# Optimization experiments

Hardware: AMD Instinct MI355X
Metric: run time of the kernel (lower is better)

## Reference

```python
import jax, jax.numpy as jnp
import numpy as np

B, SE, T, S, D, V = 64, 128, 64, 1024, 1024, 32000


def setup_inputs() -> dict:
    key = jax.random.key(0)
    ks = jax.random.split(key, 24)
    w = lambda k, shp: jax.random.normal(k, shp, jnp.float32) * 0.02
    return {
        "encoder_yts": jax.random.normal(ks[0], (B, SE, S), jnp.float32),
        "encoder_h": jax.random.normal(ks[1], (B, S), jnp.float32),
        "tgt": jax.random.randint(ks[2], (B, T), 0, V),
        "emb": w(ks[3], (V, D)),
        "asi_w": w(ks[4], (S, S)), "asi_b": jnp.zeros((S,), jnp.float32),
        "ayi_w": w(ks[5], (S, S)), "ayi_b": jnp.zeros((S,), jnp.float32),
        "aw_w": w(ks[6], (S, 1)), "aw_b": jnp.zeros((1,), jnp.float32),
        "wf_w": w(ks[7], (S, S)), "wf_b": jnp.zeros((S,), jnp.float32),
        "uf_w": w(ks[8], (D, S)), "uf_b": jnp.zeros((S,), jnp.float32),
        "wi_w": w(ks[9], (S, S)), "wi_b": jnp.zeros((S,), jnp.float32),
        "ui_w": w(ks[10], (D, S)), "ui_b": jnp.zeros((S,), jnp.float32),
        "wo_w": w(ks[11], (S, S)), "wo_b": jnp.zeros((S,), jnp.float32),
        "uo_w": w(ks[12], (D, S)), "uo_b": jnp.zeros((S,), jnp.float32),
        "wc_w": w(ks[13], (S, S)), "wc_b": jnp.zeros((S,), jnp.float32),
        "uc_w": w(ks[14], (D, S)), "uc_b": jnp.zeros((S,), jnp.float32),
        "xh_w": w(ks[15], (S, D)), "xh_b": jnp.zeros((D,), jnp.float32),
        "cls_w": w(ks[16], (D, V)), "cls_b": jnp.zeros((V,), jnp.float32),
    }


def reference(encoder_yts, encoder_h, tgt, emb,
              asi_w, asi_b, ayi_w, ayi_b, aw_w, aw_b,
              wf_w, wf_b, uf_w, uf_b, wi_w, wi_b, ui_w, ui_b,
              wo_w, wo_b, uo_w, uo_b, wc_w, wc_b, uc_w, uc_b,
              xh_w, xh_b, cls_w, cls_b):
    # Teacher-forced decode: xt at step i is the embedding of tgt[:, i].
    # Precompute attention key projection of encoder outputs: [B, SE, S]
    yts_proj = encoder_yts @ ayi_w + ayi_b
    xs = jnp.transpose(emb[tgt], (1, 0, 2))  # [T, B, D]

    def step(st, xt):
        # Additive attention (no tanh, matches source): e_ij = w^T(W si + U y)
        q = st @ asi_w + asi_b                       # [B, S]
        e = ((q[:, None, :] + yts_proj) @ aw_w)[..., 0] + aw_b[0]  # [B, SE]
        attn = jax.nn.softmax(e, axis=-1)            # [B, SE]
        ctx = jnp.einsum('be,bed->bd', attn, encoder_yts)  # [B, S] cell input
        # LSTM cell: note ct_1 is the fresh attention context each step
        ft = jax.nn.sigmoid(st @ wf_w + wf_b + xt @ uf_w + uf_b)
        it = jax.nn.sigmoid(st @ wi_w + wi_b + xt @ ui_w + ui_b)
        ot = jax.nn.sigmoid(st @ wo_w + wo_b + xt @ uo_w + uo_b)
        cbar = jnp.tanh(st @ wc_w + wc_b + xt @ uc_w + uc_b)
        ct = ft * ctx + it * cbar
        ht = ot * jnp.tanh(ct)                       # [B, S] -> next st
        logits = (ht @ xh_w + xh_b) @ cls_w + cls_b  # [B, V]
        pt = jax.nn.softmax(logits, axis=-1)
        return ht, (pt, attn)

    _, (pts, attns) = jax.lax.scan(step, encoder_h, xs)
    # [T,B,V] -> [B,T,V]; [T,B,SE] -> [B,T,SE]
    return jnp.transpose(pts, (1, 0, 2)), jnp.transpose(attns, (1, 0, 2))
```

## Files before the change

kernel.cpp:

```cpp
#include <hip/hip_runtime.h>
#include <cstdint>
#include <cstddef>

#define B_  64
#define SE_ 128
#define T_  64
#define S_  1024
#define D_  1024
#define V_  32000
#define HSLOT 65536ull

typedef __attribute__((ext_vector_type(8))) short bhalf8;
typedef __attribute__((ext_vector_type(4))) float floatx4;

__device__ __forceinline__ float sigmoidf_(float x){ return 1.0f/(1.0f+__expf(-x)); }

__device__ __forceinline__ ushort f2bf(float f){
  uint32_t u = __float_as_uint(f);
  uint32_t r = (u + 0x7fffu + ((u >> 16) & 1u)) >> 16;
  return (ushort)r;
}
__device__ __forceinline__ float bf2f(ushort h){ return __uint_as_float(((uint32_t)h) << 16); }

__device__ __forceinline__ void glds16(const ushort* g, ushort* l){
  __builtin_amdgcn_global_load_lds((const __attribute__((address_space(1))) void*)g,
                                   (__attribute__((address_space(3))) void*)l, 16, 0, 0);
}

__device__ __forceinline__ float waveRedSum(float v){
  #pragma unroll
  for (int off = 32; off; off >>= 1) v += __shfl_down(v, off, 64);
  return v;
}


__global__ void k_attnvec(const float* __restrict__ ayi_w, const float* __restrict__ aw_w,
                          float* __restrict__ v){
  int wave = (blockIdx.x * blockDim.x + threadIdx.x) >> 6;
  int lane = threadIdx.x & 63;
  if (wave >= S_) return;
  const float* row = ayi_w + (size_t)wave * S_;
  float acc = 0.f;
  #pragma unroll 4
  for (int s = lane; s < S_; s += 64) acc += row[s] * aw_w[s];
  acc = waveRedSum(acc);
  if (lane == 0) v[wave] = acc;
}

__global__ void k_scores(const float* __restrict__ yts, const float* __restrict__ v,
                         float* __restrict__ scores){
  int wave = (blockIdx.x * blockDim.x + threadIdx.x) >> 6;
  int lane = threadIdx.x & 63;
  const float* row = yts + (size_t)wave * S_;
  float acc = 0.f;
  #pragma unroll 4
  for (int s = lane; s < S_; s += 64) acc += row[s] * v[s];
  acc = waveRedSum(acc);
  if (lane == 0) scores[wave] = acc;
}

__global__ void k_attn(const float* __restrict__ scores, float* __restrict__ attnw,
                       float* __restrict__ outAttn){
  int b = blockIdx.x;
  int e = threadIdx.x;
  __shared__ float sm[128];
  float x = scores[b*SE_ + e];
  sm[e] = x; __syncthreads();
  #pragma unroll
  for (int off = 64; off; off >>= 1){
    if (e < off) sm[e] = fmaxf(sm[e], sm[e+off]);
    __syncthreads();
  }
  float m = sm[0]; __syncthreads();
  float p = __expf(x - m);
  sm[e] = p; __syncthreads();
  #pragma unroll
  for (int off = 64; off; off >>= 1){
    if (e < off) sm[e] += sm[e+off];
    __syncthreads();
  }
  float a = p / sm[0];
  attnw[b*SE_ + e] = a;
  float* dst = outAttn + (size_t)b * T_ * SE_ + e;
  #pragma unroll 4
  for (int t = 0; t < T_; ++t) dst[t*SE_] = a;
}

__global__ void k_ctx(const float* __restrict__ yts, const float* __restrict__ attnw,
                      float* __restrict__ ctx){
  int idx = blockIdx.x * blockDim.x + threadIdx.x;
  int b = idx >> 10, s = idx & (S_-1);
  const float* base = yts + (size_t)b * SE_ * S_ + s;
  const float* a = attnw + b * SE_;
  float acc = 0.f;
  #pragma unroll 8
  for (int e = 0; e < SE_; ++e) acc += a[e] * base[(size_t)e * S_];
  ctx[idx] = acc;
}


__global__ void k_transcvt(const float* __restrict__ src, ushort* __restrict__ dst,
                           int K, int N){
  __shared__ float t[32][33];
  int n0 = blockIdx.x * 32, k0 = blockIdx.y * 32;
  for (int r = threadIdx.y; r < 32; r += 8)
    t[r][threadIdx.x] = src[(size_t)(k0 + r) * N + n0 + threadIdx.x];
  __syncthreads();
  for (int r = threadIdx.y; r < 32; r += 8)
    dst[(size_t)(n0 + r) * K + k0 + threadIdx.x] = f2bf(t[threadIdx.x][r]);
}

__global__ void k_cvtrep(const float* __restrict__ src, ushort* __restrict__ Hgs){
  int i = blockIdx.x * blockDim.x + threadIdx.x;
  float4 v = ((const float4*)src)[i];
  ushort4 o; o.x = f2bf(v.x); o.y = f2bf(v.y); o.z = f2bf(v.z); o.w = f2bf(v.w);
  #pragma unroll
  for (int g = 0; g < 8; ++g) {
    size_t gbase = (g == 0) ? 0ull : (65ull + (size_t)(g-1)*8ull) * HSLOT;
    ((ushort4*)(Hgs + gbase))[i] = o;
  }
}

__global__ void k_gathercvt(const float* __restrict__ emb, const int* __restrict__ tgt,
                            ushort* __restrict__ Xb){
  int r = blockIdx.x;
  int token = tgt[((r & 63) << 6) + (r >> 6)];
  const float4* src = (const float4*)(emb + (size_t)token * D_);
  ushort* dst = Xb + (size_t)r * D_;
  int i = threadIdx.x;
  float4 v = src[i];
  ushort4 o; o.x = f2bf(v.x); o.y = f2bf(v.y); o.z = f2bf(v.z); o.w = f2bf(v.w);
  ((ushort4*)dst)[i] = o;
}

__global__ void k_packbias(const float* __restrict__ wb0, const float* __restrict__ wb1,
                           const float* __restrict__ wb2, const float* __restrict__ wb3,
                           const float* __restrict__ ub0, const float* __restrict__ ub1,
                           const float* __restrict__ ub2, const float* __restrict__ ub3,
                           float* __restrict__ dst){
  int col = blockIdx.x * blockDim.x + threadIdx.x;
  int g = col >> 10, s = col & 1023;
  const float* wb = (g==0) ? wb0 : (g==1) ? wb1 : (g==2) ? wb2 : wb3;
  const float* ub = (g==0) ? ub0 : (g==1) ? ub1 : (g==2) ? ub2 : ub3;
  dst[col] = wb[s] + ub[s];
}

template<int OUT_MODE>
__global__ __launch_bounds__(256) void k_mfma_gemm(
    const ushort* __restrict__ A, const ushort* __restrict__ BT,
    const float* __restrict__ bias, void* __restrict__ C, int M, int N)
{
  __shared__ ushort As[128*32];
  __shared__ ushort Bs[128*32];
  const int tid = threadIdx.x;
  const int lane = tid & 63, w = tid >> 6;
  const int nwg = gridDim.x * gridDim.y;
  const int L = blockIdx.y * gridDim.x + blockIdx.x;
  const int logical = (L & 7) * (nwg >> 3) + (L >> 3);
  const int by = logical / gridDim.x;
  const int bx = logical - by * gridDim.x;
  const int m0 = by * 128, n0 = bx * 128;
  const int wr = (w >> 1) * 64, wc = (w & 1) * 64;

  const int cr = (lane >> 2);
  const int ck = (lane & 3) * 8;
  const ushort* gA0 = A  + (size_t)(m0 + (2*w)*16   + cr) * 1024 + ck;
  const ushort* gA1 = A  + (size_t)(m0 + (2*w+1)*16 + cr) * 1024 + ck;
  const ushort* gB0 = BT + (size_t)(n0 + (2*w)*16   + cr) * 1024 + ck;
  const ushort* gB1 = BT + (size_t)(n0 + (2*w+1)*16 + cr) * 1024 + ck;
  ushort* lA0 = As + (2*w)*512;   ushort* lA1 = As + (2*w+1)*512;
  ushort* lB0 = Bs + (2*w)*512;   ushort* lB1 = Bs + (2*w+1)*512;

  floatx4 acc[4][4] = {};

  for (int kt = 0; kt < 1024; kt += 32) {
    glds16(gA0 + kt, lA0); glds16(gA1 + kt, lA1);
    glds16(gB0 + kt, lB0); glds16(gB1 + kt, lB1);
    __syncthreads();
    bhalf8 a[4], b[4];
    #pragma unroll
    for (int f = 0; f < 4; ++f) {
      a[f] = *(const bhalf8*)&As[(wr + f*16 + (lane & 15)) * 32 + (lane >> 4) * 8];
      b[f] = *(const bhalf8*)&Bs[(wc + f*16 + (lane & 15)) * 32 + (lane >> 4) * 8];
    }
    #pragma unroll
    for (int i = 0; i < 4; ++i)
      #pragma unroll
      for (int j = 0; j < 4; ++j)
        acc[i][j] = __builtin_amdgcn_mfma_f32_16x16x32_bf16(a[i], b[j], acc[i][j], 0, 0, 0);
    __syncthreads();
  }

  const int crow = (lane >> 4) * 4, ccol = lane & 15;
  #pragma unroll
  for (int i = 0; i < 4; ++i) {
    #pragma unroll
    for (int j = 0; j < 4; ++j) {
      int row = m0 + wr + i*16 + crow;
      int col = n0 + wc + j*16 + ccol;
      float bv = bias ? bias[col] : 0.f;
      #pragma unroll
      for (int r = 0; r < 4; ++r) {
        float v = acc[i][j][r] + bv;
        if (OUT_MODE == 0) {
          ((float*)C)[(size_t)(row + r) * N + col] = v;
        } else if (OUT_MODE == 1) {
          int rr = row + r;
          ((float*)C)[(size_t)(((rr & 63) << 6) + (rr >> 6)) * N + col] = v;
        } else {
          ((ushort*)C)[(size_t)(row + r) * N + col] = f2bf(v);
        }
      }
    }
  }
}

__global__ __launch_bounds__(512) void k_recur(
    const ushort* __restrict__ WT, const ushort* __restrict__ preb,
    const float* __restrict__ ctx, ushort* __restrict__ Hgs,
    uint* __restrict__ ready, uint* __restrict__ cnt)
{
  extern __shared__ char smem[];
  float* gbuf = (float*)smem;
  __shared__ uint sgrp, srank;
  const int tid = threadIdx.x, lane = tid & 63, w = tid >> 6;

  if (tid == 0) {
    uint xcc;
    asm volatile("s_getreg_b32 %0, hwreg(HW_REG_XCC_ID, 0, 32)" : "=s"(xcc));
    xcc &= 7u;
    sgrp = xcc;
    srank = atomicAdd(&cnt[xcc], 1u) & 31u;
  }
  __syncthreads();
  const int grp = (int)sgrp, r = (int)srank;
  const size_t gbase = (grp == 0) ? 0ull : (65ull + (size_t)(grp-1)*8ull) * HSLOT;

  const int gate = w >> 1, s16 = w & 1;
  const int colg = (gate << 10) + (r << 5) + (s16 << 4) + (lane & 15);
  const ushort* wrow = WT + ((size_t)colg << 10) + ((lane >> 4) << 3);
  bhalf8 wfrag[32];
  #pragma unroll
  for (int kk = 0; kk < 32; ++kk)
    wfrag[kk] = *(const bhalf8*)(wrow + kk*32);

  const int pb = tid >> 3;
  const int sl4 = (tid & 7) << 2;
  const float4 ctx4 = *(const float4*)(ctx + (pb << 10) + (r << 5) + sl4);

  const int arow = lane & 15;
  const int aoff = (lane >> 4) << 3;
  const int colw = (w << 4) + (lane & 15);
  uint* myflags = ready + grp * 64;

  #pragma unroll 1
  for (int t = 0; t < 64; ++t) {
    const ushort* prow = preb + (((size_t)(t*64 + pb)) << 12) + (r << 5) + sl4;
    ushort4 pf = *(const ushort4*)(prow);
    ushort4 pi = *(const ushort4*)(prow + 1024);
    ushort4 po = *(const ushort4*)(prow + 2048);
    ushort4 pc = *(const ushort4*)(prow + 3072);

    if (t > 0) {
      const uint need = (uint)t;
      floatx4 j0 = {}, j1 = {}, j2 = {}, j3 = {};
      for (;;) {
        uint v = __hip_atomic_load(myflags + (lane & 31), __ATOMIC_RELAXED,
                                   __HIP_MEMORY_SCOPE_AGENT);
        if (__all(v >= need)) break;
        #pragma unroll
        for (int hh = 0; hh < 8; ++hh) {
          j0 = __builtin_amdgcn_mfma_f32_16x16x32_bf16(wfrag[hh],    wfrag[hh+8],  j0, 0,0,0);
          j1 = __builtin_amdgcn_mfma_f32_16x16x32_bf16(wfrag[hh+8],  wfrag[hh+16], j1, 0,0,0);
          j2 = __builtin_amdgcn_mfma_f32_16x16x32_bf16(wfrag[hh+16], wfrag[hh+24], j2, 0,0,0);
          j3 = __builtin_amdgcn_mfma_f32_16x16x32_bf16(wfrag[hh+24], wfrag[hh],    j3, 0,0,0);
        }
      }
      asm volatile("" :: "v"(j0[0]), "v"(j1[0]), "v"(j2[0]), "v"(j3[0]));
      __syncthreads();
      asm volatile("" ::: "memory");
    }

    const ushort* Hrd = Hgs + gbase + (size_t)(grp == 0 ? t : (t & 7)) * HSLOT;
    floatx4 acc[4] = {};
    #pragma unroll
    for (int kk = 0; kk < 32; ++kk) {
      #pragma unroll
      for (int i = 0; i < 4; ++i) {
        bhalf8 a = *(const bhalf8*)(Hrd + ((i*16 + arow) << 10) + kk*32 + aoff);
        acc[i] = __builtin_amdgcn_mfma_f32_16x16x32_bf16(a, wfrag[kk], acc[i], 0, 0, 0);
      }
    }

    #pragma unroll
    for (int i = 0; i < 4; ++i) {
      #pragma unroll
      for (int rr = 0; rr < 4; ++rr)
        gbuf[(i*16 + ((lane >> 4) << 2) + rr)*132 + colw] = acc[i][rr];
    }
    __syncthreads();

    {
      const float* gb = gbuf + pb*132;
      float h[4];
      const ushort* pfp = (const ushort*)&pf; const ushort* pip = (const ushort*)&pi;
      const ushort* pop = (const ushort*)&po; const ushort* pcp = (const ushort*)&pc;
      const float* cxp = (const float*)&ctx4;
      #pragma unroll
      for (int c = 0; c < 4; ++c) {
        float fv = gb[      sl4 + c] + bf2f(pfp[c]);
        float iv = gb[32  + sl4 + c] + bf2f(pip[c]);
        float ov = gb[64  + sl4 + c] + bf2f(pop[c]);
        float cv = gb[96  + sl4 + c] + bf2f(pcp[c]);
        float ct = sigmoidf_(fv) * cxp[c] + sigmoidf_(iv) * tanhf(cv);
        h[c] = sigmoidf_(ov) * tanhf(ct);
      }
      ushort4 hv; hv.x = f2bf(h[0]); hv.y = f2bf(h[1]); hv.z = f2bf(h[2]); hv.w = f2bf(h[3]);
      ushort* Hwr = Hgs + gbase + (size_t)(grp == 0 ? (t+1) : ((t+1) & 7)) * HSLOT;
      *(ushort4*)(Hwr + (pb << 10) + (r << 5) + sl4) = hv;
    }
    __syncthreads();
    if (tid == 0)
      __hip_atomic_store(myflags + r, (uint)(t + 1), __ATOMIC_RELAXED,
                         __HIP_MEMORY_SCOPE_AGENT);
  }
}

__global__ __launch_bounds__(256) void k_softmaxV(float* __restrict__ out){
  extern __shared__ float rowbuf[];
  int r = blockIdx.x;
  float4* p = (float4*)(out + (size_t)r * V_);
  float4* rb = (float4*)rowbuf;
  int tid = threadIdx.x;
  float m = -1e30f, ssum = 0.f;
  for (int i = tid; i < 8000; i += 256) {
    float4 v = p[i];
    rb[i] = v;
    float m4 = fmaxf(fmaxf(v.x, v.y), fmaxf(v.z, v.w));
    float mn = fmaxf(m, m4);
    ssum = ssum * __expf(m - mn)
         + __expf(v.x - mn) + __expf(v.y - mn) + __expf(v.z - mn) + __expf(v.w - mn);
    m = mn;
  }
  __shared__ float ms[256], ss[256];
  ms[tid] = m; ss[tid] = ssum; __syncthreads();
  #pragma unroll
  for (int off = 128; off; off >>= 1) {
    if (tid < off) {
      float m2 = fmaxf(ms[tid], ms[tid+off]);
      ss[tid] = ss[tid]*__expf(ms[tid]-m2) + ss[tid+off]*__expf(ms[tid+off]-m2);
      ms[tid] = m2;
    }
    __syncthreads();
  }
  float M = ms[0];
  float inv = 1.0f / ss[0];
  for (int i = tid; i < 8000; i += 256) {
    float4 v = rb[i];
    v.x = __expf(v.x - M) * inv; v.y = __expf(v.y - M) * inv;
    v.z = __expf(v.z - M) * inv; v.w = __expf(v.w - M) * inv;
    p[i] = v;
  }
}


extern "C" void kernel_launch(void* const* d_in, const int* in_sizes, int n_in,
                              void* d_out, int out_size, void* d_ws, size_t ws_size,
                              hipStream_t stream){
  const float* yts   = (const float*)d_in[0];
  const float* enc_h = (const float*)d_in[1];
  const int*   tgt   = (const int*)d_in[2];
  const float* emb   = (const float*)d_in[3];
  const float* ayi_w = (const float*)d_in[6];
  const float* aw_w  = (const float*)d_in[8];
  const float* wf_w = (const float*)d_in[10]; const float* wf_b = (const float*)d_in[11];
  const float* uf_w = (const float*)d_in[12]; const float* uf_b = (const float*)d_in[13];
  const float* wi_w = (const float*)d_in[14]; const float* wi_b = (const float*)d_in[15];
  const float* ui_w = (const float*)d_in[16]; const float* ui_b = (const float*)d_in[17];
  const float* wo_w = (const float*)d_in[18]; const float* wo_b = (const float*)d_in[19];
  const float* uo_w = (const float*)d_in[20]; const float* uo_b = (const float*)d_in[21];
  const float* wc_w = (const float*)d_in[22]; const float* wc_b = (const float*)d_in[23];
  const float* uc_w = (const float*)d_in[24]; const float* uc_b = (const float*)d_in[25];
  const float* xh_w = (const float*)d_in[26]; const float* xh_b = (const float*)d_in[27];
  const float* cls_w= (const float*)d_in[28]; const float* cls_b= (const float*)d_in[29];

  float* out = (float*)d_out;
  float* outAttn = out + (size_t)B_ * T_ * V_;

  char* wsb = (char*)d_ws;
  size_t off = 0;
  auto alloc = [&](size_t bytes)->char*{
    char* p = wsb + off; off += (bytes + 255) & ~(size_t)255; return p;
  };
  ushort* clsT  = (ushort*)alloc((size_t)V_ * 1024 * 2);
  ushort* xhT   = (ushort*)alloc((size_t)1024 * 1024 * 2);
  ushort* WcatT = (ushort*)alloc((size_t)4096 * 1024 * 2);
  ushort* UcatT = (ushort*)alloc((size_t)4096 * 1024 * 2);
  float*  biasU = (float*)alloc(4096 * 4);
  float*  vvec  = (float*)alloc(S_ * 4);
  float*  scores= (float*)alloc(B_ * SE_ * 4);
  float*  attnw = (float*)alloc(B_ * SE_ * 4);
  float*  ctx   = (float*)alloc(B_ * S_ * 4);
  uint*   ready = (uint*)alloc(8 * 64 * 4);
  uint*   cnt   = (uint*)alloc(256);
  ushort* Xb    = (ushort*)alloc((size_t)4096 * 1024 * 2);
  ushort* preb  = (ushort*)alloc((size_t)4096 * 4096 * 2);
  ushort* Hgs   = (ushort*)alloc((65ull + 7ull*8ull) * HSLOT * 2);
  if (off > ws_size) return;
  ushort* Zb = Xb;

  dim3 tb(32, 8);
  k_transcvt<<<dim3(V_/32, 32), tb, 0, stream>>>(cls_w, clsT, 1024, V_);
  k_transcvt<<<dim3(32, 32), tb, 0, stream>>>(xh_w, xhT, 1024, 1024);
  k_transcvt<<<dim3(32, 32), tb, 0, stream>>>(wf_w, WcatT + 0u*1048576u, 1024, 1024);
  k_transcvt<<<dim3(32, 32), tb, 0, stream>>>(wi_w, WcatT + 1u*1048576u, 1024, 1024);
  k_transcvt<<<dim3(32, 32), tb, 0, stream>>>(wo_w, WcatT + 2u*1048576u, 1024, 1024);
  k_transcvt<<<dim3(32, 32), tb, 0, stream>>>(wc_w, WcatT + 3u*1048576u, 1024, 1024);
  k_transcvt<<<dim3(32, 32), tb, 0, stream>>>(uf_w, UcatT + 0u*1048576u, 1024, 1024);
  k_transcvt<<<dim3(32, 32), tb, 0, stream>>>(ui_w, UcatT + 1u*1048576u, 1024, 1024);
  k_transcvt<<<dim3(32, 32), tb, 0, stream>>>(uo_w, UcatT + 2u*1048576u, 1024, 1024);
  k_transcvt<<<dim3(32, 32), tb, 0, stream>>>(uc_w, UcatT + 3u*1048576u, 1024, 1024);
  k_packbias<<<16, 256, 0, stream>>>(wf_b, wi_b, wo_b, wc_b, uf_b, ui_b, uo_b, uc_b, biasU);
  k_cvtrep<<<64, 256, 0, stream>>>(enc_h, Hgs);
  k_gathercvt<<<4096, 256, 0, stream>>>(emb, tgt, Xb);

  k_attnvec<<<256, 256, 0, stream>>>(ayi_w, aw_w, vvec);
  k_scores<<<2048, 256, 0, stream>>>(yts, vvec, scores);
  k_attn<<<64, 128, 0, stream>>>(scores, attnw, outAttn);
  k_ctx<<<256, 256, 0, stream>>>(yts, attnw, ctx);

  k_mfma_gemm<2><<<dim3(32, 32), 256, 0, stream>>>(Xb, UcatT, biasU, preb, 4096, 4096);

  hipMemsetAsync(ready, 0, 8 * 64 * 4, stream);
  hipMemsetAsync(cnt, 0, 256, stream);
  {
    void* args[] = { (void*)&WcatT, (void*)&preb, (void*)&ctx, (void*)&Hgs,
                     (void*)&ready, (void*)&cnt };
    hipLaunchCooperativeKernel((void*)k_recur, dim3(256), dim3(512), args, 86016, stream);
  }

  k_mfma_gemm<2><<<dim3(8, 32), 256, 0, stream>>>(Hgs + HSLOT, xhT, xh_b, Zb, 4096, 1024);
  k_mfma_gemm<1><<<dim3(V_/128, 32), 256, 0, stream>>>(Zb, clsT, cls_b, out, 4096, V_);
  k_softmaxV<<<4096, 256, 128000, stream>>>(out);
}
```

Baseline: 3.109 ms.

## Run recurrence on one XCD group and spin only one wave on flags

Previously all 8 XCD groups of 32 blocks each ran the full recurrence redundantly on replicated hidden-state buffers. Now only group 0 computes, and the other 7 groups spin on a done flag while issuing dummy MFMAs, then exit. Inside a block, only wave 0 polls the global ready flags and publishes the step through LDS, while the other waves spin on LDS with dummy MFMAs, replacing a block-wide __syncthreads. This is meant to cut redundant memory traffic and polling contention, possibly letting clocks or L2 serve the active group better. The risk is that the idle groups' dummy MFMA spinning still draws power, and the LDS handoff adds a little latency per step.

```diff
diff --git a/kernel.cpp b/kernel.cpp
--- a/kernel.cpp
+++ b/kernel.cpp
@@ -110,15 +110,12 @@
     dst[(size_t)(n0 + r) * K + k0 + threadIdx.x] = f2bf(t[threadIdx.x][r]);
 }
 
-__global__ void k_cvtrep(const float* __restrict__ src, ushort* __restrict__ Hgs){
+__global__ void k_cvt(const float* __restrict__ src, ushort* __restrict__ dst, int n4){
   int i = blockIdx.x * blockDim.x + threadIdx.x;
+  if (i >= n4) return;
   float4 v = ((const float4*)src)[i];
   ushort4 o; o.x = f2bf(v.x); o.y = f2bf(v.y); o.z = f2bf(v.z); o.w = f2bf(v.w);
-  #pragma unroll
-  for (int g = 0; g < 8; ++g) {
-    size_t gbase = (g == 0) ? 0ull : (65ull + (size_t)(g-1)*8ull) * HSLOT;
-    ((ushort4*)(Hgs + gbase))[i] = o;
-  }
+  ((ushort4*)dst)[i] = o;
 }
 
 __global__ void k_gathercvt(const float* __restrict__ emb, const int* __restrict__ tgt,
@@ -218,11 +215,11 @@
 __global__ __launch_bounds__(512) void k_recur(
     const ushort* __restrict__ WT, const ushort* __restrict__ preb,
     const float* __restrict__ ctx, ushort* __restrict__ Hgs,
-    uint* __restrict__ ready, uint* __restrict__ cnt)
+    uint* __restrict__ ready, uint* __restrict__ cnt, uint* __restrict__ done)
 {
   extern __shared__ char smem[];
   float* gbuf = (float*)smem;
-  __shared__ uint sgrp, srank;
+  __shared__ uint sgrp, srank, lds_step;
   const int tid = threadIdx.x, lane = tid & 63, w = tid >> 6;
 
   if (tid == 0) {
@@ -231,10 +228,10 @@
     xcc &= 7u;
     sgrp = xcc;
     srank = atomicAdd(&cnt[xcc], 1u) & 31u;
+    lds_step = 0u;
   }
   __syncthreads();
   const int grp = (int)sgrp, r = (int)srank;
-  const size_t gbase = (grp == 0) ? 0ull : (65ull + (size_t)(grp-1)*8ull) * HSLOT;
 
   const int gate = w >> 1, s16 = w & 1;
   const int colg = (gate << 10) + (r << 5) + (s16 << 4) + (lane & 15);
@@ -244,14 +241,30 @@
   for (int kk = 0; kk < 32; ++kk)
     wfrag[kk] = *(const bhalf8*)(wrow + kk*32);
 
+  if (grp != 0) {
+    floatx4 j0 = {}, j1 = {}, j2 = {}, j3 = {};
+    for (;;) {
+      uint v = __hip_atomic_load(done + (lane & 31), __ATOMIC_RELAXED,
+                                 __HIP_MEMORY_SCOPE_SYSTEM);
+      if (__all(v != 0u)) break;
+      #pragma unroll 4
+      for (int it = 0; it < 128; ++it) {
+        j0 = __builtin_amdgcn_mfma_f32_16x16x32_bf16(wfrag[it & 7],        wfrag[(it & 7) + 8],  j0, 0,0,0);
+        j1 = __builtin_amdgcn_mfma_f32_16x16x32_bf16(wfrag[(it & 7) + 8],  wfrag[(it & 7) + 16], j1, 0,0,0);
+        j2 = __builtin_amdgcn_mfma_f32_16x16x32_bf16(wfrag[(it & 7) + 16], wfrag[(it & 7) + 24], j2, 0,0,0);
+        j3 = __builtin_amdgcn_mfma_f32_16x16x32_bf16(wfrag[(it & 7) + 24], wfrag[it & 7],        j3, 0,0,0);
+      }
+    }
+    asm volatile("" :: "v"(j0[0]), "v"(j1[0]), "v"(j2[0]), "v"(j3[0]));
+    return;
+  }
+
   const int pb = tid >> 3;
   const int sl4 = (tid & 7) << 2;
   const float4 ctx4 = *(const float4*)(ctx + (pb << 10) + (r << 5) + sl4);
-
   const int arow = lane & 15;
   const int aoff = (lane >> 4) << 3;
   const int colw = (w << 4) + (lane & 15);
-  uint* myflags = ready + grp * 64;
 
   #pragma unroll 1
   for (int t = 0; t < 64; ++t) {
@@ -262,26 +275,34 @@
     ushort4 pc = *(const ushort4*)(prow + 3072);
 
     if (t > 0) {
-      const uint need = (uint)t;
-      floatx4 j0 = {}, j1 = {}, j2 = {}, j3 = {};
-      for (;;) {
-        uint v = __hip_atomic_load(myflags + (lane & 31), __ATOMIC_RELAXED,
-                                   __HIP_MEMORY_SCOPE_AGENT);
-        if (__all(v >= need)) break;
-        #pragma unroll
-        for (int hh = 0; hh < 8; ++hh) {
-          j0 = __builtin_amdgcn_mfma_f32_16x16x32_bf16(wfrag[hh],    wfrag[hh+8],  j0, 0,0,0);
-          j1 = __builtin_amdgcn_mfma_f32_16x16x32_bf16(wfrag[hh+8],  wfrag[hh+16], j1, 0,0,0);
-          j2 = __builtin_amdgcn_mfma_f32_16x16x32_bf16(wfrag[hh+16], wfrag[hh+24], j2, 0,0,0);
-          j3 = __builtin_amdgcn_mfma_f32_16x16x32_bf16(wfrag[hh+24], wfrag[hh],    j3, 0,0,0);
+      if (w == 0) {
+        const uint need = (uint)t;
+        for (;;) {
+          uint v = __hip_atomic_load(ready + (lane & 31), __ATOMIC_RELAXED,
+                                     __HIP_MEMORY_SCOPE_AGENT);
+          if (__all(v >= need)) break;
         }
+        if (lane == 0)
+          __hip_atomic_store(&lds_step, (uint)t, __ATOMIC_RELAXED,
+                             __HIP_MEMORY_SCOPE_WORKGROUP);
+      } else {
+        floatx4 j0 = {}, j1 = {}, j2 = {}, j3 = {};
+        while (__hip_atomic_load(&lds_step, __ATOMIC_RELAXED,
+                                 __HIP_MEMORY_SCOPE_WORKGROUP) < (uint)t) {
+          #pragma unroll
+          for (int hh = 0; hh < 8; ++hh) {
+            j0 = __builtin_amdgcn_mfma_f32_16x16x32_bf16(wfrag[hh],    wfrag[hh+8],  j0, 0,0,0);
+            j1 = __builtin_amdgcn_mfma_f32_16x16x32_bf16(wfrag[hh+8],  wfrag[hh+16], j1, 0,0,0);
+            j2 = __builtin_amdgcn_mfma_f32_16x16x32_bf16(wfrag[hh+16], wfrag[hh+24], j2, 0,0,0);
+            j3 = __builtin_amdgcn_mfma_f32_16x16x32_bf16(wfrag[hh+24], wfrag[hh],    j3, 0,0,0);
+          }
+        }
+        asm volatile("" :: "v"(j0[0]), "v"(j1[0]), "v"(j2[0]), "v"(j3[0]));
       }
-      asm volatile("" :: "v"(j0[0]), "v"(j1[0]), "v"(j2[0]), "v"(j3[0]));
-      __syncthreads();
       asm volatile("" ::: "memory");
     }
 
-    const ushort* Hrd = Hgs + gbase + (size_t)(grp == 0 ? t : (t & 7)) * HSLOT;
+    const ushort* Hrd = Hgs + (size_t)t * HSLOT;
     floatx4 acc[4] = {};
     #pragma unroll
     for (int kk = 0; kk < 32; ++kk) {
@@ -316,14 +337,15 @@
         h[c] = sigmoidf_(ov) * tanhf(ct);
       }
       ushort4 hv; hv.x = f2bf(h[0]); hv.y = f2bf(h[1]); hv.z = f2bf(h[2]); hv.w = f2bf(h[3]);
-      ushort* Hwr = Hgs + gbase + (size_t)(grp == 0 ? (t+1) : ((t+1) & 7)) * HSLOT;
-      *(ushort4*)(Hwr + (pb << 10) + (r << 5) + sl4) = hv;
+      *(ushort4*)(Hgs + (size_t)(t+1) * HSLOT + (pb << 10) + (r << 5) + sl4) = hv;
     }
     __syncthreads();
     if (tid == 0)
-      __hip_atomic_store(myflags + r, (uint)(t + 1), __ATOMIC_RELAXED,
+      __hip_atomic_store(ready + r, (uint)(t + 1), __ATOMIC_RELAXED,
                          __HIP_MEMORY_SCOPE_AGENT);
   }
+  if (tid == 0)
+    __hip_atomic_store(done + r, 1u, __ATOMIC_RELAXED, __HIP_MEMORY_SCOPE_SYSTEM);
 }
 
 __global__ __launch_bounds__(256) void k_softmaxV(float* __restrict__ out){
@@ -401,11 +423,12 @@
   float*  scores= (float*)alloc(B_ * SE_ * 4);
   float*  attnw = (float*)alloc(B_ * SE_ * 4);
   float*  ctx   = (float*)alloc(B_ * S_ * 4);
-  uint*   ready = (uint*)alloc(8 * 64 * 4);
+  uint*   ready = (uint*)alloc(256);
   uint*   cnt   = (uint*)alloc(256);
+  uint*   done  = (uint*)alloc(256);
   ushort* Xb    = (ushort*)alloc((size_t)4096 * 1024 * 2);
   ushort* preb  = (ushort*)alloc((size_t)4096 * 4096 * 2);
-  ushort* Hgs   = (ushort*)alloc((65ull + 7ull*8ull) * HSLOT * 2);
+  ushort* Hgs   = (ushort*)alloc(65ull * HSLOT * 2);
   if (off > ws_size) return;
   ushort* Zb = Xb;
 
@@ -421,7 +444,7 @@
   k_transcvt<<<dim3(32, 32), tb, 0, stream>>>(uo_w, UcatT + 2u*1048576u, 1024, 1024);
   k_transcvt<<<dim3(32, 32), tb, 0, stream>>>(uc_w, UcatT + 3u*1048576u, 1024, 1024);
   k_packbias<<<16, 256, 0, stream>>>(wf_b, wi_b, wo_b, wc_b, uf_b, ui_b, uo_b, uc_b, biasU);
-  k_cvtrep<<<64, 256, 0, stream>>>(enc_h, Hgs);
+  k_cvt<<<64, 256, 0, stream>>>(enc_h, Hgs, 16384);
   k_gathercvt<<<4096, 256, 0, stream>>>(emb, tgt, Xb);
 
   k_attnvec<<<256, 256, 0, stream>>>(ayi_w, aw_w, vvec);
@@ -431,11 +454,12 @@
 
   k_mfma_gemm<2><<<dim3(32, 32), 256, 0, stream>>>(Xb, UcatT, biasU, preb, 4096, 4096);
 
-  hipMemsetAsync(ready, 0, 8 * 64 * 4, stream);
+  hipMemsetAsync(ready, 0, 256, stream);
   hipMemsetAsync(cnt, 0, 256, stream);
+  hipMemsetAsync(done, 0, 256, stream);
   {
     void* args[] = { (void*)&WcatT, (void*)&preb, (void*)&ctx, (void*)&Hgs,
-                     (void*)&ready, (void*)&cnt };
+                     (void*)&ready, (void*)&cnt, (void*)&done };
     hipLaunchCooperativeKernel((void*)k_recur, dim3(256), dim3(512), args, 86016, stream);
   }
 
```

Result: slower. 3.991 ms (+28.4%).
